# Performance work log

Measured on AMD Instinct MI355X. Metric: run time of the kernel, lower is better.

The kernel has to match this reference:

```python
import jax, jax.numpy as jnp
import numpy as np

H = 128  # LSTM hidden size
EPS = 1e-5  # BatchNorm eps


def _lstm_scan(seq, Wih, Whh, bih, bhh, h0, c0):
    """Unbatched LSTM over seq [N, D] with torch gate order (i, f, g, o)."""
    b = bih + bhh

    def step(carry, xt):
        h, c = carry
        gates = xt @ Wih.T + h @ Whh.T + b  # [4H]
        i, f, g, o = jnp.split(gates, 4)
        i = jax.nn.sigmoid(i)
        f = jax.nn.sigmoid(f)
        g = jnp.tanh(g)
        o = jax.nn.sigmoid(o)
        c = f * c + i * g
        h = o * jnp.tanh(c)
        return (h, c), h

    (h, c), ys = jax.lax.scan(step, (h0, c0), seq)
    return ys  # [N, H]


def _lstm_forward(x, Wih, Whh, bih, bhh, h0, c0):
    # Faithful to TypeNet.lstm_forward: for each timestep i, x[:, i] ([B, D])
    # is fed to nn.LSTM as an UNBATCHED sequence of length B, and the final
    # (hx, cx) carries into the next timestep column. This is equivalent to a
    # single scan over the flattened [T*B, D] sequence (column-major order).
    B, T, D = x.shape
    seq = jnp.transpose(x, (1, 0, 2)).reshape(T * B, D)
    ys = _lstm_scan(seq, Wih, Whh, bih, bhh, h0, c0)
    return ys.reshape(T, B, H)  # matches torch.stack(output, dim=0)


def _bn(x, gamma, beta):
    # BatchNorm1d in training-mode math over (N, C, L): stats over dims (0, 2).
    mean = x.mean(axis=(0, 2), keepdims=True)
    var = ((x - mean) ** 2).mean(axis=(0, 2), keepdims=True)
    return gamma[None, :, None] * (x - mean) * jax.lax.rsqrt(var + EPS) + beta[None, :, None]


def _single_forward(x, branch, g1, b1, Wih1, Whh1, bih1, bhh1,
                    g2, b2, Wih2, Whh2, bih2, bhh2, h0s, c0s):
    x = _bn(x, g1, b1)                                        # [128, 16, 3]
    x = _lstm_forward(x, Wih1, Whh1, bih1, bhh1,
                      h0s[2 * branch], c0s[2 * branch])       # [16, 128, 128]
    # dropout layers are identity (p = 0.0)
    x = _bn(x, g2, b2)                                        # C = 128 at dim 1
    x = _lstm_forward(x, Wih2, Whh2, bih2, bhh2,
                      h0s[2 * branch + 1], c0s[2 * branch + 1])  # [128, 16, 128]
    return x


def setup_inputs() -> dict:
    key = jax.random.key(0)
    ks = jax.random.split(key, 12)
    s = 1.0 / np.sqrt(H)  # torch LSTM init scale
    return {
        "x": jax.random.normal(ks[0], (128, 48, 3), dtype=jnp.float32),
        "g1": jnp.ones((16,), jnp.float32),
        "b1": jnp.zeros((16,), jnp.float32),
        "Wih1": jax.random.uniform(ks[1], (4 * H, 3), jnp.float32, -s, s),
        "Whh1": jax.random.uniform(ks[2], (4 * H, H), jnp.float32, -s, s),
        "bih1": jax.random.uniform(ks[3], (4 * H,), jnp.float32, -s, s),
        "bhh1": jax.random.uniform(ks[4], (4 * H,), jnp.float32, -s, s),
        "g2": jnp.ones((H,), jnp.float32),
        "b2": jnp.zeros((H,), jnp.float32),
        "Wih2": jax.random.uniform(ks[5], (4 * H, H), jnp.float32, -s, s),
        "Whh2": jax.random.uniform(ks[6], (4 * H, H), jnp.float32, -s, s),
        "bih2": jax.random.uniform(ks[7], (4 * H,), jnp.float32, -s, s),
        "bhh2": jax.random.uniform(ks[8], (4 * H,), jnp.float32, -s, s),
        # 6 LSTM calls (2 layers x 3 branches), each with its own random init state
        "h0s": jax.random.normal(ks[9], (6, H), dtype=jnp.float32),
        "c0s": jax.random.normal(ks[10], (6, H), dtype=jnp.float32),
    }


def reference(x, g1, b1, Wih1, Whh1, bih1, bhh1,
              g2, b2, Wih2, Whh2, bih2, bhh2, h0s, c0s):
    d1, d2, d3 = jnp.split(x, 3, axis=1)  # each [128, 16, 3]
    args = (g1, b1, Wih1, Whh1, bih1, bhh1, g2, b2, Wih2, Whh2, bih2, bhh2, h0s, c0s)
    anchor = _single_forward(d1, 0, *args)
    positive = _single_forward(d2, 1, *args)
    negative = _single_forward(d3, 2, *args)
    return anchor, positive, negative  # each [128, 16, 128]
```

## Files before the change

kernel.cpp:

```cpp
#include <hip/hip_runtime.h>


typedef _Float16 half4_t __attribute__((ext_vector_type(4)));
typedef _Float16 half8 __attribute__((ext_vector_type(8)));
typedef float float4_t __attribute__((ext_vector_type(4)));
typedef int int4_t __attribute__((ext_vector_type(4)));

#define LOG2E 1.44269504f

__device__ __forceinline__ float fast_rcp(float x) { return __builtin_amdgcn_rcpf(x); }
__device__ __forceinline__ float exp2b(float x) { return __builtin_amdgcn_exp2f(x); }

#define QBCAST(x, pat)                                                        \
  __int_as_float(__builtin_amdgcn_update_dpp(0, __float_as_int(x), (pat),     \
                                             0xF, 0xF, true))

__device__ __forceinline__ void lds_barrier() {
  asm volatile("s_waitcnt lgkmcnt(0)\n\ts_barrier" ::: "memory");
}

__host__ __device__ __forceinline__ int ridx0_of(int j) {
  return (j >> 4) * 64 + ((j >> 2) & 3) * 16 + (j & 3) * 4;
}

__global__ __launch_bounds__(128) void bn1_kernel(const float* __restrict__ x,
                                                  const float* __restrict__ g1,
                                                  const float* __restrict__ b1,
                                                  float* __restrict__ xbn) {
  const int br = blockIdx.x >> 4;
  const int t  = blockIdx.x & 15;
  const int b  = threadIdx.x;
  const float* px = x + (b * 48 + br * 16 + t) * 3;
  const float v0 = px[0], v1 = px[1], v2 = px[2];
  float s  = v0 + v1 + v2;
  float ss = v0 * v0 + v1 * v1 + v2 * v2;
  for (int off = 32; off; off >>= 1) {
    s  += __shfl_down(s, off);
    ss += __shfl_down(ss, off);
  }
  __shared__ float red[4];
  if ((threadIdx.x & 63) == 0) {
    red[(threadIdx.x >> 6) * 2]     = s;
    red[(threadIdx.x >> 6) * 2 + 1] = ss;
  }
  __syncthreads();
  const float S = red[0] + red[2], SS = red[1] + red[3];
  const float mean = S * (1.0f / 384.0f);
  const float var  = SS * (1.0f / 384.0f) - mean * mean;
  const float rstd = rsqrtf(var + 1e-5f);
  const float a  = g1[t] * rstd;
  const float sh = b1[t] - mean * a;
  float* dst = xbn + br * 6144 + (t * 128 + b) * 3;
  dst[0] = v0 * a + sh;
  dst[1] = v1 * a + sh;
  dst[2] = v2 * a + sh;
}

__global__ __launch_bounds__(256) void g1x_kernel(const float* __restrict__ xbn,
                                                  const float* __restrict__ Wih1,
                                                  const float* __restrict__ bih1,
                                                  const float* __restrict__ bhh1,
                                                  _Float16* __restrict__ G1x) {
  const int br = blockIdx.x >> 10;
  const int sp = blockIdx.x & 1023;
  const int s  = sp * 2 + (threadIdx.x >> 7);
  const int j  = threadIdx.x & 127;
  const float* px = xbn + br * 6144 + s * 3;
  const float x0 = px[0], x1 = px[1], x2 = px[2];
  _Float16* base =
      G1x + ((size_t)(br * 128 + (s >> 4)) * 512 + ridx0_of(j)) * 16 + (s & 15);
#pragma unroll
  for (int g = 0; g < 4; ++g) {
    const int row = g * 128 + j;
    float a = bih1[row] + bhh1[row] + Wih1[row * 3] * x0 +
              Wih1[row * 3 + 1] * x1 + Wih1[row * 3 + 2] * x2;
    a *= (g == 2) ? (2.0f * LOG2E) : LOG2E;
    base[g * 16] = (_Float16)a;
  }
}

__global__ __launch_bounds__(256) void bn2stats_kernel(const float* __restrict__ H1,
                                                       float* __restrict__ stats) {
  const int br = blockIdx.x >> 7;
  const int ch = blockIdx.x & 127;
  const float* base = H1 + (size_t)br * 262144 + ch * 128;
  float s = 0.f, ss = 0.f;
  for (int k = threadIdx.x; k < 2048; k += 256) {
    const int t1 = k >> 7, h = k & 127;
    const float v = base[t1 * 16384 + h];
    s += v;
    ss += v * v;
  }
  for (int off = 32; off; off >>= 1) {
    s  += __shfl_down(s, off);
    ss += __shfl_down(ss, off);
  }
  __shared__ float red[8];
  if ((threadIdx.x & 63) == 0) {
    red[(threadIdx.x >> 6) * 2]     = s;
    red[(threadIdx.x >> 6) * 2 + 1] = ss;
  }
  __syncthreads();
  if (threadIdx.x == 0) {
    const float S  = red[0] + red[2] + red[4] + red[6];
    const float SS = red[1] + red[3] + red[5] + red[7];
    const float mean = S * (1.0f / 2048.0f);
    const float var  = SS * (1.0f / 2048.0f) - mean * mean;
    stats[(br * 128 + ch) * 2]     = mean;
    stats[(br * 128 + ch) * 2 + 1] = rsqrtf(var + 1e-5f);
  }
}

__global__ __launch_bounds__(256) void g2x_kernel(
    const float* __restrict__ H1, const float* __restrict__ stats,
    const float* __restrict__ g2, const float* __restrict__ b2v,
    const float* __restrict__ Wih2, const float* __restrict__ bih2,
    const float* __restrict__ bhh2, _Float16* __restrict__ G2x) {
  const int br = blockIdx.x >> 7;
  const int t2 = blockIdx.x & 127;
  __shared__ float xh[2048];
  __shared__ float wt[64 * 129];
  const float mean = stats[(br * 128 + t2) * 2];
  const float rstd = stats[(br * 128 + t2) * 2 + 1];
  const float a  = g2[t2] * rstd;
  const float sh = b2v[t2] - mean * a;
  for (int e = threadIdx.x; e < 2048; e += 256) {
    const int b2 = e >> 7, d = e & 127;
    xh[e] = H1[(size_t)br * 262144 + (size_t)(b2 * 128 + t2) * 128 + d] * a + sh;
  }
  const int gl  = threadIdx.x & 63;
  const int b2b = (threadIdx.x >> 6) * 4;
  for (int gt = 0; gt < 8; ++gt) {
    __syncthreads();
    for (int e = threadIdx.x; e < 8192; e += 256)
      wt[(e >> 7) * 129 + (e & 127)] = Wih2[gt * 8192 + e];
    __syncthreads();
    float a0 = 0.f, a1 = 0.f, a2 = 0.f, a3 = 0.f;
    for (int d = 0; d < 128; ++d) {
      const float w = wt[gl * 129 + d];
      a0 += w * xh[(b2b + 0) * 128 + d];
      a1 += w * xh[(b2b + 1) * 128 + d];
      a2 += w * xh[(b2b + 2) * 128 + d];
      a3 += w * xh[(b2b + 3) * 128 + d];
    }
    const int g    = gt * 64 + gl;
    const int gate = g >> 7;
    const int jj   = g & 127;
    const int ri   = ridx0_of(jj) + gate;
    const float bb = bih2[g] + bhh2[g];
    const float mul = (gate == 2) ? (2.0f * LOG2E) : LOG2E;
    _Float16* dst = G2x + ((size_t)(br * 128 + t2) * 512 + ri) * 16 + b2b;
    *reinterpret_cast<half4_t*>(dst) =
        half4_t{(_Float16)((a0 + bb) * mul), (_Float16)((a1 + bb) * mul),
                (_Float16)((a2 + bb) * mul), (_Float16)((a3 + bb) * mul)};
  }
}

__global__ __launch_bounds__(512, 1) void lstm_kernel(
    const float* __restrict__ Whh, const float* __restrict__ h0s,
    const float* __restrict__ c0s, const _Float16* __restrict__ Gx,
    float* __restrict__ outp, int layer) {
  const int br   = blockIdx.x;
  const int tid  = threadIdx.x;
  const int wave = tid >> 6;
  const int lane = tid & 63;
  const int quad = lane >> 4;
  const int l15  = lane & 15;
  const int gate = l15 & 3;
  const int rr   = l15 >> 2;
  const int j    = wave * 16 + quad * 4 + rr;
  const bool rb0 = (rr & 1) != 0;
  const bool rb1 = (rr & 2) != 0;
  const bool gb0 = (gate & 1) != 0;
  const bool gb1 = (gate & 2) != 0;
  const float scg = (gate == 2) ? 2.0f : 1.0f;
  const float Bcg = (gate == 2) ? 2.0f : 1.0f;

  __shared__ __align__(16) signed char h_sh[2][128];
  __shared__ float rowscale[512];
  __shared__ __align__(16) float h0f[128];

  int4_t afrag[4][2];
#pragma unroll
  for (int g = 0; g < 4; ++g) {
    const int row = g * 128 + wave * 16 + l15;
    const float4_t* wr = (const float4_t*)(Whh + row * 128);
    float m = 1e-8f;
    for (int k4 = 0; k4 < 32; ++k4) {
      const float4_t v = wr[k4];
      m = fmaxf(m, fmaxf(fmaxf(fabsf(v[0]), fabsf(v[1])),
                         fmaxf(fabsf(v[2]), fabsf(v[3]))));
    }
    if (quad == 0) rowscale[row] = m;
    const float inv = 127.0f / m;
#pragma unroll
    for (int t = 0; t < 2; ++t) {
      int4_t f;
#pragma unroll
      for (int w = 0; w < 4; ++w) {
        int word = 0;
#pragma unroll
        for (int b = 0; b < 4; ++b) {
          const int k = t * 64 + quad * 16 + w * 4 + b;
          const int q = (int)__builtin_rintf(Whh[row * 128 + k] * inv);
          word |= (q & 255) << (8 * b);
        }
        f[w] = word;
      }
      afrag[g][t] = f;
    }
  }

  const int slot = 2 * br + layer;
  float c = c0s[slot * 128 + j];
  if (tid < 128) {
    const float h0 = h0s[slot * 128 + tid];
    h0f[tid] = h0;
    float qf = __builtin_rintf(h0 * 127.0f);
    qf = fminf(fmaxf(qf, -127.0f), 127.0f);
    h_sh[0][tid] = (signed char)(int)qf;
  }

  const half8* gq = (const half8*)Gx;
  half8 curA = gq[((size_t)(br * 128) * 512 + tid) * 2];
  half8 curB = gq[((size_t)(br * 128) * 512 + tid) * 2 + 1];
  float* const obase = outp + (size_t)br * 262144;

  const int4_t zi = {0, 0, 0, 0};
  __syncthreads();

  const float s_own =
      rowscale[gate * 128 + j] * (LOG2E / (127.0f * 127.0f)) * scg;

  float exact0;
  {
    const int rowo = gate * 128 + j;
    const float4_t* wr4 = (const float4_t*)(Whh + rowo * 128);
    const float4_t* h04 = (const float4_t*)h0f;
    float e0 = 0.f, e1 = 0.f;
#pragma unroll 8
    for (int k4 = 0; k4 < 32; k4 += 2) {
      const float4_t a0 = wr4[k4],     b0 = h04[k4];
      const float4_t a1 = wr4[k4 + 1], b1 = h04[k4 + 1];
      e0 = __builtin_fmaf(a0[0], b0[0], e0);
      e0 = __builtin_fmaf(a0[1], b0[1], e0);
      e0 = __builtin_fmaf(a0[2], b0[2], e0);
      e0 = __builtin_fmaf(a0[3], b0[3], e0);
      e1 = __builtin_fmaf(a1[0], b1[0], e1);
      e1 = __builtin_fmaf(a1[1], b1[1], e1);
      e1 = __builtin_fmaf(a1[2], b1[2], e1);
      e1 = __builtin_fmaf(a1[3], b1[3], e1);
    }
    exact0 = (e0 + e1) * (LOG2E * scg);
  }

  if (((wave ^ (wave >> 2)) & 1) != 0) __builtin_amdgcn_s_setprio(2);

  float qres = 0.f;

  for (int chk = 0; chk < 128; ++chk) {
    const int chn = (chk < 127) ? chk + 1 : 127;
    const size_t nrec = ((size_t)(br * 128 + chn) * 512 + tid) * 2;
    const half8 nA = gq[nrec], nB = gq[nrec + 1];

#pragma unroll
    for (int u = 0; u < 16; ++u) {
      const signed char* hs = h_sh[u & 1];
      const int4_t b0 = *(const int4_t*)(hs + quad * 16);
      const int4_t b1 = *(const int4_t*)(hs + 64 + quad * 16);

      const float pre = (float)((u < 8) ? curA[u] : curB[u - 8]);

      int4_t acc[4];
#pragma unroll
      for (int g = 0; g < 4; ++g)
        acc[g] = __builtin_amdgcn_mfma_i32_16x16x64_i8(afrag[g][0], b0, zi, 0, 0, 0);
#pragma unroll
      for (int g = 0; g < 4; ++g)
        acc[g] = __builtin_amdgcn_mfma_i32_16x16x64_i8(afrag[g][1], b1, acc[g], 0, 0, 0);

      int e0, e1, e2, e3;
      {
        int x, y;
        x = rb0 ? acc[0][1] : acc[0][0]; y = rb0 ? acc[0][3] : acc[0][2];
        e0 = rb1 ? y : x;
        x = rb0 ? acc[1][1] : acc[1][0]; y = rb0 ? acc[1][3] : acc[1][2];
        e1 = rb1 ? y : x;
        x = rb0 ? acc[2][1] : acc[2][0]; y = rb0 ? acc[2][3] : acc[2][2];
        e2 = rb1 ? y : x;
        x = rb0 ? acc[3][1] : acc[3][0]; y = rb0 ? acc[3][3] : acc[3][2];
        e3 = rb1 ? y : x;
      }
      const int eA = gb0 ? e1 : e0;
      const int eB = gb0 ? e3 : e2;
      const int ei = gb1 ? eB : eA;

      float a = __builtin_fmaf((float)ei, s_own, pre);
      if (u == 0 && chk == 0) a = exact0 + pre;

      const float act = __builtin_fmaf(-Bcg, fast_rcp(1.0f + exp2b(a)), 1.0f);

      const float iv = QBCAST(act, 0x00);
      const float fv = QBCAST(act, 0x55);
      const float gv = QBCAST(act, 0xAA);
      const float ov = QBCAST(act, 0xFF);

      c = fv * c + iv * gv;
      const float t  = __builtin_fmaf(
          -2.0f, fast_rcp(1.0f + exp2b(c * 2.88539008f)), 1.0f);
      const float hv = ov * t;

      if (gate == 0) {
        const float t2 = __builtin_fmaf(hv, 127.0f, qres);
        float qf = __builtin_rintf(t2);
        qf = __builtin_amdgcn_fmed3f(qf, -127.0f, 127.0f);
        qres = t2 - qf;
        h_sh[(u + 1) & 1][j] = (signed char)(int)qf;
        float* orow = obase + (size_t)(chk * 16 + u) * 128;
        orow[j] = hv;
      }
      lds_barrier();
    }

    curA = nA;
    curB = nB;
  }
}

extern "C" void kernel_launch(void* const* d_in, const int* in_sizes, int n_in,
                              void* d_out, int out_size, void* d_ws, size_t ws_size,
                              hipStream_t stream) {
  const float* x    = (const float*)d_in[0];
  const float* g1   = (const float*)d_in[1];
  const float* b1   = (const float*)d_in[2];
  const float* Wih1 = (const float*)d_in[3];
  const float* Whh1 = (const float*)d_in[4];
  const float* bih1 = (const float*)d_in[5];
  const float* bhh1 = (const float*)d_in[6];
  const float* g2   = (const float*)d_in[7];
  const float* b2   = (const float*)d_in[8];
  const float* Wih2 = (const float*)d_in[9];
  const float* Whh2 = (const float*)d_in[10];
  const float* bih2 = (const float*)d_in[11];
  const float* bhh2 = (const float*)d_in[12];
  const float* h0s  = (const float*)d_in[13];
  const float* c0s  = (const float*)d_in[14];

  float* ws   = (float*)d_ws;
  float* xbn  = ws;
  float* H1b  = ws + 18432;
  float* st   = ws + 18432 + 786432;
  _Float16* G1xb = (_Float16*)(ws + 805632);
  _Float16* G2xb = (_Float16*)(ws + 2378496);
  float* outp = (float*)d_out;

  bn1_kernel<<<48, 128, 0, stream>>>(x, g1, b1, xbn);
  g1x_kernel<<<3072, 256, 0, stream>>>(xbn, Wih1, bih1, bhh1, G1xb);
  lstm_kernel<<<3, 512, 0, stream>>>(Whh1, h0s, c0s, G1xb, H1b, 0);
  bn2stats_kernel<<<384, 256, 0, stream>>>(H1b, st);
  g2x_kernel<<<384, 256, 0, stream>>>(H1b, st, g2, b2, Wih2, bih2, bhh2, G2xb);
  lstm_kernel<<<3, 512, 0, stream>>>(Whh2, h0s, c0s, G2xb, outp, 1);
}
```

Measured before the change: 1.516 ms.

## Replace int8 MFMA recurrent matvec with per-thread v_dot4 over register-resident weights

Each thread now keeps its own quantized Whh row (32 packed int8 words) in registers and computes the recurrent gate dot product with 32 v_dot4_i32_i8 instructions over the full broadcast h vector read from LDS. This replaces 8 MFMA ops per step plus lane-select extraction, with the aim of cutting MFMA latency on the serial critical path. The wave priority setting is also removed. In exchange, each thread does many more LDS reads and VALU ops per step, and register pressure rises.

```diff
diff --git a/kernel.cpp b/kernel.cpp
--- a/kernel.cpp
+++ b/kernel.cpp
@@ -10,6 +10,16 @@
 
 __device__ __forceinline__ float fast_rcp(float x) { return __builtin_amdgcn_rcpf(x); }
 __device__ __forceinline__ float exp2b(float x) { return __builtin_amdgcn_exp2f(x); }
+
+__device__ __forceinline__ int dot4i8(int a, int b, int c) {
+#if __has_builtin(__builtin_amdgcn_sdot4)
+  return __builtin_amdgcn_sdot4(a, b, c, false);
+#else
+  int d;
+  asm("v_dot4_i32_i8 %0, %1, %2, %3" : "=v"(d) : "v"(a), "v"(b), "v"(c));
+  return d;
+#endif
+}
 
 #define QBCAST(x, pat)                                                        \
   __int_as_float(__builtin_amdgcn_update_dpp(0, __float_as_int(x), (pat),     \
@@ -169,47 +179,34 @@
   const int gate = l15 & 3;
   const int rr   = l15 >> 2;
   const int j    = wave * 16 + quad * 4 + rr;
-  const bool rb0 = (rr & 1) != 0;
-  const bool rb1 = (rr & 2) != 0;
-  const bool gb0 = (gate & 1) != 0;
-  const bool gb1 = (gate & 2) != 0;
+  const int row  = gate * 128 + j;
   const float scg = (gate == 2) ? 2.0f : 1.0f;
   const float Bcg = (gate == 2) ? 2.0f : 1.0f;
 
   __shared__ __align__(16) signed char h_sh[2][128];
-  __shared__ float rowscale[512];
   __shared__ __align__(16) float h0f[128];
 
-  int4_t afrag[4][2];
-#pragma unroll
-  for (int g = 0; g < 4; ++g) {
-    const int row = g * 128 + wave * 16 + l15;
-    const float4_t* wr = (const float4_t*)(Whh + row * 128);
-    float m = 1e-8f;
-    for (int k4 = 0; k4 < 32; ++k4) {
-      const float4_t v = wr[k4];
-      m = fmaxf(m, fmaxf(fmaxf(fabsf(v[0]), fabsf(v[1])),
-                         fmaxf(fabsf(v[2]), fabsf(v[3]))));
+  const float4_t* wr = (const float4_t*)(Whh + row * 128);
+  float m = 1e-8f;
+  for (int k4 = 0; k4 < 32; ++k4) {
+    const float4_t v = wr[k4];
+    m = fmaxf(m, fmaxf(fmaxf(fabsf(v[0]), fabsf(v[1])),
+                       fmaxf(fabsf(v[2]), fabsf(v[3]))));
+  }
+  const float inv = 127.0f / m;
+  int wq[32];
+#pragma unroll
+  for (int d = 0; d < 32; ++d) {
+    const float4_t v = wr[d];
+    int word = 0;
+#pragma unroll
+    for (int b = 0; b < 4; ++b) {
+      const int q = (int)__builtin_rintf(v[b] * inv);
+      word |= (q & 255) << (8 * b);
     }
-    if (quad == 0) rowscale[row] = m;
-    const float inv = 127.0f / m;
-#pragma unroll
-    for (int t = 0; t < 2; ++t) {
-      int4_t f;
-#pragma unroll
-      for (int w = 0; w < 4; ++w) {
-        int word = 0;
-#pragma unroll
-        for (int b = 0; b < 4; ++b) {
-          const int k = t * 64 + quad * 16 + w * 4 + b;
-          const int q = (int)__builtin_rintf(Whh[row * 128 + k] * inv);
-          word |= (q & 255) << (8 * b);
-        }
-        f[w] = word;
-      }
-      afrag[g][t] = f;
-    }
-  }
+    wq[d] = word;
+  }
+  const float s_own = m * (LOG2E / (127.0f * 127.0f)) * scg;
 
   const int slot = 2 * br + layer;
   float c = c0s[slot * 128 + j];
@@ -226,22 +223,16 @@
   half8 curB = gq[((size_t)(br * 128) * 512 + tid) * 2 + 1];
   float* const obase = outp + (size_t)br * 262144;
 
-  const int4_t zi = {0, 0, 0, 0};
   __syncthreads();
-
-  const float s_own =
-      rowscale[gate * 128 + j] * (LOG2E / (127.0f * 127.0f)) * scg;
 
   float exact0;
   {
-    const int rowo = gate * 128 + j;
-    const float4_t* wr4 = (const float4_t*)(Whh + rowo * 128);
     const float4_t* h04 = (const float4_t*)h0f;
     float e0 = 0.f, e1 = 0.f;
 #pragma unroll 8
     for (int k4 = 0; k4 < 32; k4 += 2) {
-      const float4_t a0 = wr4[k4],     b0 = h04[k4];
-      const float4_t a1 = wr4[k4 + 1], b1 = h04[k4 + 1];
+      const float4_t a0 = wr[k4],     b0 = h04[k4];
+      const float4_t a1 = wr[k4 + 1], b1 = h04[k4 + 1];
       e0 = __builtin_fmaf(a0[0], b0[0], e0);
       e0 = __builtin_fmaf(a0[1], b0[1], e0);
       e0 = __builtin_fmaf(a0[2], b0[2], e0);
@@ -254,8 +245,6 @@
     exact0 = (e0 + e1) * (LOG2E * scg);
   }
 
-  if (((wave ^ (wave >> 2)) & 1) != 0) __builtin_amdgcn_s_setprio(2);
-
   float qres = 0.f;
 
   for (int chk = 0; chk < 128; ++chk) {
@@ -265,35 +254,28 @@
 
 #pragma unroll
     for (int u = 0; u < 16; ++u) {
-      const signed char* hs = h_sh[u & 1];
-      const int4_t b0 = *(const int4_t*)(hs + quad * 16);
-      const int4_t b1 = *(const int4_t*)(hs + 64 + quad * 16);
+      const int4_t* hv4 = (const int4_t*)h_sh[u & 1];
+      int hdw[32];
+#pragma unroll
+      for (int r = 0; r < 8; ++r) {
+        const int4_t hh = hv4[r];
+        hdw[r * 4 + 0] = hh[0];
+        hdw[r * 4 + 1] = hh[1];
+        hdw[r * 4 + 2] = hh[2];
+        hdw[r * 4 + 3] = hh[3];
+      }
 
       const float pre = (float)((u < 8) ? curA[u] : curB[u - 8]);
 
-      int4_t acc[4];
-#pragma unroll
-      for (int g = 0; g < 4; ++g)
-        acc[g] = __builtin_amdgcn_mfma_i32_16x16x64_i8(afrag[g][0], b0, zi, 0, 0, 0);
-#pragma unroll
-      for (int g = 0; g < 4; ++g)
-        acc[g] = __builtin_amdgcn_mfma_i32_16x16x64_i8(afrag[g][1], b1, acc[g], 0, 0, 0);
-
-      int e0, e1, e2, e3;
-      {
-        int x, y;
-        x = rb0 ? acc[0][1] : acc[0][0]; y = rb0 ? acc[0][3] : acc[0][2];
-        e0 = rb1 ? y : x;
-        x = rb0 ? acc[1][1] : acc[1][0]; y = rb0 ? acc[1][3] : acc[1][2];
-        e1 = rb1 ? y : x;
-        x = rb0 ? acc[2][1] : acc[2][0]; y = rb0 ? acc[2][3] : acc[2][2];
-        e2 = rb1 ? y : x;
-        x = rb0 ? acc[3][1] : acc[3][0]; y = rb0 ? acc[3][3] : acc[3][2];
-        e3 = rb1 ? y : x;
+      int a0 = 0, a1 = 0, a2 = 0, a3 = 0;
+#pragma unroll
+      for (int i = 0; i < 8; ++i) {
+        a0 = dot4i8(wq[i],      hdw[i],      a0);
+        a1 = dot4i8(wq[8 + i],  hdw[8 + i],  a1);
+        a2 = dot4i8(wq[16 + i], hdw[16 + i], a2);
+        a3 = dot4i8(wq[24 + i], hdw[24 + i], a3);
       }
-      const int eA = gb0 ? e1 : e0;
-      const int eB = gb0 ? e3 : e2;
-      const int ei = gb1 ? eB : eA;
+      const int ei = (a0 + a1) + (a2 + a3);
 
       float a = __builtin_fmaf((float)ei, s_own, pre);
       if (u == 0 && chk == 0) a = exact0 + pre;
```

Result: slower. 1.687 ms (+11.3%).
